# Kernel optimization log

Hardware: AMD Instinct MI355X
Metric: run time of the kernel (lower is better)

## Reference

```python
import jax, jax.numpy as jnp
import numpy as np

B, C1, C2, H, W = 8, 256, 512, 56, 56

def setup_inputs() -> dict:
    key = jax.random.key(0)
    k1, k2, k3, k4, k5 = jax.random.split(key, 5)
    return {
        "x1": jax.random.normal(k1, (B, C1, H, W), dtype=jnp.float32),
        "x2": jax.random.normal(k2, (B, C2, H, W), dtype=jnp.float32),
        "W_proj": jax.random.normal(k3, (C1, C2), dtype=jnp.float32) * (1.0 / np.sqrt(C2)),
        "b_proj": jax.random.normal(k4, (C1,), dtype=jnp.float32) * 0.01,
        "gamma": jax.random.normal(k5, (1,), dtype=jnp.float32) * 0.1,
    }

def reference(x1, x2, W_proj, b_proj, gamma):
    b, c, h, w = x1.shape
    n = h * w
    # 1x1 conv projection C2 -> C1
    x2p = jnp.einsum('oc,bchw->bohw', W_proj, x2) + b_proj[None, :, None, None]
    query = x1.reshape(b, c, n).transpose(0, 2, 1)   # [B, N, C]
    key_ = x2p.reshape(b, c, n)                      # [B, C, N]
    value = x2p.reshape(b, c, n).transpose(0, 2, 1)  # [B, N, C]
    energy = jnp.einsum('bnc,bcm->bnm', query, key_)  # [B, N, N]
    # inverted-energy softmax: max - energy, then softmax over last dim
    energy_new = jnp.max(energy, axis=-1, keepdims=True) - energy
    attention = jax.nn.softmax(energy_new, axis=-1)
    out = jnp.einsum('bnm,bmc->bnc', attention, value)  # [B, N, C]
    out = out.transpose(0, 2, 1).reshape(b, c, h, w)
    return gamma[0] * out + x1
```

## Files before the change

### kernel.cpp

```cpp
#include <hip/hip_runtime.h>
#include <hip/hip_bf16.h>

#define C1 256
#define C2 512
#define NSP 3136
#define NT 98
#define LOG2E 1.44269504f
#define THR2 11.5453f

typedef __attribute__((ext_vector_type(8))) short bf16x8;
typedef __attribute__((ext_vector_type(4))) float f32x4;

__device__ __forceinline__ ushort f2b(float f) {
  __hip_bfloat16 h = __float2bfloat16(f);
  return *reinterpret_cast<ushort*>(&h);
}
__device__ __forceinline__ float b2f(ushort u) {
  union { unsigned int i; float f; } v; v.i = ((unsigned int)u) << 16; return v.f;
}
__device__ __forceinline__ float fexp2(float x) {
  return __builtin_amdgcn_exp2f(x);
}
__device__ __forceinline__ void gload16(const ushort* g, ushort* l) {
  __builtin_amdgcn_global_load_lds(
      (const __attribute__((address_space(1))) void*)g,
      (__attribute__((address_space(3))) void*)l, 16, 0, 0);
}
__device__ __forceinline__ void block_bar() {
  asm volatile("" ::: "memory");
  __builtin_amdgcn_s_barrier();
  asm volatile("" ::: "memory");
}

__global__ __launch_bounds__(256) void k_wtf(const float* __restrict__ W,
                                             ushort* __restrict__ Wf) {
  int ot = blockIdx.x;
  int tid = threadIdx.x;
  int lane = tid & 63, l15 = lane & 15, g = (lane >> 4) & 3;
  int cc0 = (tid >> 6) * 4;
  const float* src = W + (size_t)(ot * 16 + l15) * C2 + g * 8;
#pragma unroll
  for (int k = 0; k < 4; k++) {
    int cc = cc0 + k;
    float4 u0 = *reinterpret_cast<const float4*>(src + cc * 32);
    float4 u1 = *reinterpret_cast<const float4*>(src + cc * 32 + 4);
    bf16x8 v;
    v[0] = (short)f2b(u0.x); v[1] = (short)f2b(u0.y);
    v[2] = (short)f2b(u0.z); v[3] = (short)f2b(u0.w);
    v[4] = (short)f2b(u1.x); v[5] = (short)f2b(u1.y);
    v[6] = (short)f2b(u1.z); v[7] = (short)f2b(u1.w);
    *reinterpret_cast<bf16x8*>(Wf + ((size_t)(ot * 16 + cc)) * 512 + lane * 8) = v;
  }
}

__global__ __launch_bounds__(256) void k_x1t(const float* __restrict__ x1,
                                             ushort* __restrict__ x1t) {
  __shared__ float t[32][33];
  int b = blockIdx.z;
  int n0 = blockIdx.x * 32;
  int c0 = blockIdx.y * 32;
  int tid = threadIdx.x;
  int r = tid >> 3, q = (tid & 7) * 4;
  const float* src = x1 + ((size_t)b * C1 + (c0 + r)) * NSP + n0 + q;
  float4 v = *reinterpret_cast<const float4*>(src);
  t[r][q] = v.x; t[r][q + 1] = v.y; t[r][q + 2] = v.z; t[r][q + 3] = v.w;
  __syncthreads();
  ushort4 o;
  o.x = f2b(t[q + 0][r] * LOG2E); o.y = f2b(t[q + 1][r] * LOG2E);
  o.z = f2b(t[q + 2][r] * LOG2E); o.w = f2b(t[q + 3][r] * LOG2E);
  *reinterpret_cast<ushort4*>(x1t + ((size_t)b * NSP + n0 + r) * C1 + c0 + q) = o;
}

__global__ __launch_bounds__(256) void k_x2f(const float* __restrict__ x2,
                                             ushort* __restrict__ x2f) {
  __shared__ float t[32][33];
  int b = blockIdx.z;
  int n0 = blockIdx.x * 32;
  int cc = blockIdx.y;
  int c0 = cc * 32;
  int tid = threadIdx.x;
  int r = tid >> 3, q = (tid & 7) * 4;
  const float* src = x2 + ((size_t)b * C2 + (c0 + r)) * NSP + n0 + q;
  float4 v = *reinterpret_cast<const float4*>(src);
  t[r][q] = v.x; t[r][q + 1] = v.y; t[r][q + 2] = v.z; t[r][q + 3] = v.w;
  __syncthreads();
  int l15 = tid & 15, g = (tid >> 4) & 3, sub = tid >> 6;
  int ntl = sub & 1, ih = sub >> 1;
  int nl = ntl * 16 + l15;
  int cl = g * 8 + ih * 4;
  ushort4 o;
  o.x = f2b(t[cl + 0][nl]); o.y = f2b(t[cl + 1][nl]);
  o.z = f2b(t[cl + 2][nl]); o.w = f2b(t[cl + 3][nl]);
  int nt16 = (n0 >> 4) + ntl;
  *reinterpret_cast<ushort4*>(
      x2f + (((size_t)b * 196 + nt16) * 16 + cc) * 512 + (size_t)(tid & 63) * 8 + ih * 4) = o;
}

__global__ __launch_bounds__(256) void k_proj(const ushort* __restrict__ Wf,
    const ushort* __restrict__ x2f, const float* __restrict__ bias,
    ushort* __restrict__ Kf, ushort* __restrict__ Vf) {
  __shared__ __align__(16) ushort WL[2][8][512];
  __shared__ __align__(16) ushort XL[2][4][512];
  int bid = blockIdx.x;
  int b = bid & 7;
  int tq = bid >> 3;
  int oh = tq & 1;
  int nt = tq >> 1;
  int tid = threadIdx.x;
  int w = tid >> 6, lane = tid & 63, l15 = lane & 15, g = lane >> 4;
  int wq = w >> 1, wn = w & 1;
  int ot0 = oh * 8;
  int nt0 = nt * 4;

  auto stage = [&](int buf, int cc) {
#pragma unroll
    for (int j = 0; j < 3; j++) {
      int chunk = w * 3 + j;
      if (chunk < 8) {
        gload16(Wf + ((size_t)(ot0 + chunk) * 16 + cc) * 512 + lane * 8,
                &WL[buf][chunk][0]);
      } else {
        gload16(x2f + (((size_t)b * 196 + nt0 + (chunk - 8)) * 16 + cc) * 512 + lane * 8,
                &XL[buf][chunk - 8][0]);
      }
    }
  };

  f32x4 zero = {0.f, 0.f, 0.f, 0.f};
  f32x4 acc[4][2];
#pragma unroll
  for (int a = 0; a < 4; a++)
#pragma unroll
    for (int v = 0; v < 2; v++) acc[a][v] = zero;

  stage(0, 0);
  __syncthreads();

  for (int cc = 0; cc < 16; ++cc) {
    int cur = cc & 1;
    if (cc < 15) stage(cur ^ 1, cc + 1);
    bf16x8 A[4], Bf[2];
#pragma unroll
    for (int a = 0; a < 4; a++)
      A[a] = *reinterpret_cast<const bf16x8*>(&WL[cur][wq * 4 + a][lane * 8]);
#pragma unroll
    for (int v = 0; v < 2; v++)
      Bf[v] = *reinterpret_cast<const bf16x8*>(&XL[cur][wn * 2 + v][lane * 8]);
#pragma unroll
    for (int a = 0; a < 4; a++)
#pragma unroll
      for (int v = 0; v < 2; v++)
        acc[a][v] = __builtin_amdgcn_mfma_f32_16x16x32_bf16(A[a], Bf[v], acc[a][v], 0, 0, 0);
    __syncthreads();
  }

  int obase = oh * 128 + wq * 64;
  float4 bias4[4];
#pragma unroll
  for (int a = 0; a < 4; a++)
    bias4[a] = *reinterpret_cast<const float4*>(&bias[obase + a * 16 + g * 4]);

  int gk = (g & 1) * 4;
#pragma unroll
  for (int a = 0; a < 4; a++) {
    int laneK = (((2 * a + (g >> 1)) & 3) << 4) | l15;
    size_t oK = (size_t)(oh * 4 + wq * 2 + (a >> 1));
#pragma unroll
    for (int v = 0; v < 2; v++) {
      int nK = nt * 4 + wn * 2 + v;
      ushort4 st;
      st.x = f2b(acc[a][v][0] + bias4[a].x);
      st.y = f2b(acc[a][v][1] + bias4[a].y);
      st.z = f2b(acc[a][v][2] + bias4[a].z);
      st.w = f2b(acc[a][v][3] + bias4[a].w);
      *reinterpret_cast<ushort4*>(
          Kf + ((((size_t)b * 196 + nK) * 8 + oK) * 64 + laneK) * 8 + gk) = st;
    }
  }
  int nV = nt * 2 + wn;
#pragma unroll
  for (int v = 0; v < 2; v++) {
    int gv = ((v * 2 + (l15 >> 3)) & 3) << 4;
    int iV = l15 & 7;
#pragma unroll
    for (int a = 0; a < 4; a++) {
      int cs = oh * 8 + wq * 4 + a;
      size_t basev = ((((size_t)b * 98 + nV) * 16 + cs) * 64 + gv) * 8 + iV;
      const float* bp4 = reinterpret_cast<const float*>(&bias4[a]);
#pragma unroll
      for (int r = 0; r < 4; r++)
        Vf[basev + (size_t)(g * 4 + r) * 8] = f2b(acc[a][v][r] + bp4[r]);
    }
  }
}

__global__ __launch_bounds__(256, 3) void k_attn_s(
    const ushort* __restrict__ x1t, const ushort* __restrict__ Kf,
    const ushort* __restrict__ Vf,
    ushort* __restrict__ Po, float* __restrict__ Mv, float* __restrict__ Lv) {
  __shared__ __align__(16) ushort Kt[2][8192];
  __shared__ __align__(16) ushort Vt[8192];
  __shared__ __align__(16) ushort Plds[4][16][36];
  int bid = blockIdx.x;
  int x = bid & 7;
  int j = bid >> 3;
  int s = (4802 * j) / 96;
  int e = (4802 * (j + 1)) / 96;
  int tid = threadIdx.x;
  int w = tid >> 6;
  int lane = tid & 63;
  int l15 = lane & 15;
  int g = lane >> 4;
  int nloc = w * 16 + g * 4;

  const ushort* kg = Kf + (size_t)x * 196 * 8 * 512;
  const ushort* vg = Vf + (size_t)x * 98 * 16 * 512;
  int soff = w * 2048;

  f32x4 zero = {0.f, 0.f, 0.f, 0.f};
  f32x4 O[16];
  f32x4 O17 = zero;
  float M[4];
  bf16x8 qf[8];
  bf16x8 onesf;
#pragma unroll
  for (int i = 0; i < 8; i++) onesf[i] = (short)0x3F80;

  auto resetacc = [&]() {
#pragma unroll
    for (int i = 0; i < 16; i++) O[i] = zero;
    O17 = zero;
#pragma unroll
    for (int r = 0; r < 4; r++) M[r] = -3.0e38f;
  };
  auto loadQ = [&](int u) {
    const ushort* qb = x1t + ((size_t)x * NSP + u * 64 + w * 16 + l15) * C1 + g * 8;
#pragma unroll
    for (int cc = 0; cc < 8; cc++)
      qf[cc] = *reinterpret_cast<const bf16x8*>(qb + cc * 32);
  };

  int u = s / 98;
  int kv = s - u * 98;
  loadQ(u);
  resetacc();
  {
    const ushort* ks = kg + (size_t)kv * 8192 + soff + lane * 8;
#pragma unroll
    for (int jj = 0; jj < 4; ++jj) gload16(ks + jj * 512, &Kt[0][soff] + jj * 512);
  }
  asm volatile("s_waitcnt vmcnt(0)" ::: "memory");
  block_bar();

  int cur = 0;
  for (int i = s; i < e; ++i) {
    {
      const ushort* vs = vg + (size_t)kv * 8192 + soff + lane * 8;
#pragma unroll
      for (int jj = 0; jj < 4; ++jj) gload16(vs + jj * 512, &Vt[soff] + jj * 512);
    }
    asm volatile("" ::: "memory");
    if (i + 1 < e) {
      int kvn = (kv == 97) ? 0 : kv + 1;
      const ushort* ks = kg + (size_t)kvn * 8192 + soff + lane * 8;
#pragma unroll
      for (int jj = 0; jj < 4; ++jj) gload16(ks + jj * 512, &Kt[cur ^ 1][soff] + jj * 512);
    }
    asm volatile("" ::: "memory");

    f32x4 s0a = zero, s0b = zero, s1a = zero, s1b = zero;
    const ushort* kb = &Kt[cur][0];
    __builtin_amdgcn_s_setprio(1);
#pragma unroll
    for (int cc = 0; cc < 8; cc += 2) {
      bf16x8 k00 = *reinterpret_cast<const bf16x8*>(kb + ((size_t)cc * 64 + lane) * 8);
      bf16x8 k10 = *reinterpret_cast<const bf16x8*>(kb + ((size_t)(8 + cc) * 64 + lane) * 8);
      bf16x8 k01 = *reinterpret_cast<const bf16x8*>(kb + ((size_t)(cc + 1) * 64 + lane) * 8);
      bf16x8 k11 = *reinterpret_cast<const bf16x8*>(kb + ((size_t)(9 + cc) * 64 + lane) * 8);
      s0a = __builtin_amdgcn_mfma_f32_16x16x32_bf16(qf[cc], k00, s0a, 0, 0, 0);
      s1a = __builtin_amdgcn_mfma_f32_16x16x32_bf16(qf[cc], k10, s1a, 0, 0, 0);
      s0b = __builtin_amdgcn_mfma_f32_16x16x32_bf16(qf[cc + 1], k01, s0b, 0, 0, 0);
      s1b = __builtin_amdgcn_mfma_f32_16x16x32_bf16(qf[cc + 1], k11, s1b, 0, 0, 0);
    }
    __builtin_amdgcn_s_setprio(0);

    float a0[4], a1[4], tmax[4];
#pragma unroll
    for (int r = 0; r < 4; r++) {
      a0[r] = -(s0a[r] + s0b[r]);
      a1[r] = -(s1a[r] + s1b[r]);
      float mx = fmaxf(a0[r], a1[r]);
      mx = fmaxf(mx, __shfl_xor(mx, 1));
      mx = fmaxf(mx, __shfl_xor(mx, 2));
      mx = fmaxf(mx, __shfl_xor(mx, 4));
      mx = fmaxf(mx, __shfl_xor(mx, 8));
      tmax[r] = mx;
    }
    float d01 = fmaxf(tmax[0] - M[0], tmax[1] - M[1]);
    float d23 = fmaxf(tmax[2] - M[2], tmax[3] - M[3]);
    if (__any(fmaxf(d01, d23) > THR2)) {
      float scv[4];
#pragma unroll
      for (int r = 0; r < 4; r++) {
        float nm = fmaxf(M[r], tmax[r]);
        scv[r] = fexp2(M[r] - nm);
        M[r] = nm;
      }
#pragma unroll
      for (int i2 = 0; i2 < 16; i2++) {
#pragma unroll
        for (int r = 0; r < 4; r++) O[i2][r] *= scv[r];
      }
#pragma unroll
      for (int r = 0; r < 4; r++) O17[r] *= scv[r];
    }
#pragma unroll
    for (int r = 0; r < 4; r++) {
      Plds[w][g * 4 + r][l15] = f2b(fexp2(a0[r] - M[r]));
      Plds[w][g * 4 + r][16 + l15] = f2b(fexp2(a1[r] - M[r]));
    }

    if (i + 1 < e) { asm volatile("s_waitcnt vmcnt(4)" ::: "memory"); }
    else           { asm volatile("s_waitcnt vmcnt(0)" ::: "memory"); }
    block_bar();

    asm volatile("s_waitcnt lgkmcnt(0)" ::: "memory");
    bf16x8 pf = *reinterpret_cast<const bf16x8*>(&Plds[w][l15][g * 8]);
    __builtin_amdgcn_s_setprio(1);
#pragma unroll
    for (int cs = 0; cs < 16; ++cs) {
      bf16x8 vf = *reinterpret_cast<const bf16x8*>(&Vt[0] + ((size_t)cs * 64 + lane) * 8);
      O[cs] = __builtin_amdgcn_mfma_f32_16x16x32_bf16(pf, vf, O[cs], 0, 0, 0);
    }
    O17 = __builtin_amdgcn_mfma_f32_16x16x32_bf16(pf, onesf, O17, 0, 0, 0);
    __builtin_amdgcn_s_setprio(0);

    asm volatile("s_waitcnt vmcnt(0)" ::: "memory");
    block_bar();
    cur ^= 1;

    if ((i + 1 == e) || (kv == 97)) {
      int firstj = (9408 * u + 95) / 4802;
      int slot = (x * 49 + u) * 3 + (j - firstj);
#pragma unroll
      for (int cs = 0; cs < 16; cs++) {
        int c = cs * 16 + l15;
        ushort4 st;
        st.x = f2b(O[cs][0]); st.y = f2b(O[cs][1]);
        st.z = f2b(O[cs][2]); st.w = f2b(O[cs][3]);
        *reinterpret_cast<ushort4*>(Po + ((size_t)slot * 256 + c) * 64 + nloc) = st;
      }
      if (l15 == 0) {
#pragma unroll
        for (int r = 0; r < 4; r++) {
          Mv[(size_t)slot * 64 + nloc + r] = M[r];
          Lv[(size_t)slot * 64 + nloc + r] = O17[r];
        }
      }
      if (i + 1 < e && kv == 97) { u += 1; loadQ(u); resetacc(); }
    }
    kv = (kv == 97) ? 0 : kv + 1;
  }
}

__global__ __launch_bounds__(256) void k_comb3(
    const ushort* __restrict__ Po, const float* __restrict__ Mv,
    const float* __restrict__ Lv, const float* __restrict__ x1,
    const float* __restrict__ gamma, float* __restrict__ out) {
  int bid = blockIdx.x;
  int x = bid & 7;
  int u = bid >> 3;
  int tid = threadIdx.x;
  int n = tid & 63;
  int c0 = (tid >> 6) * 64;
  int firstj = (9408 * u + 95) / 4802;
  int lastj = (96 * (98 * u + 97) + 95) / 4802;
  int np = lastj - firstj + 1;
  size_t base = (size_t)(x * 49 + u) * 3;
  bool has2 = (np >= 3);

  float M0 = Mv[(base + 0) * 64 + n];
  float M1 = Mv[(base + 1) * 64 + n];
  float M2 = has2 ? Mv[(base + 2) * 64 + n] : -3.0e38f;
  float L0 = Lv[(base + 0) * 64 + n];
  float L1 = Lv[(base + 1) * 64 + n];
  float L2 = has2 ? Lv[(base + 2) * 64 + n] : 0.f;
  float Mg = fmaxf(fmaxf(M0, M1), M2);
  float w0 = fexp2(M0 - Mg), w1 = fexp2(M1 - Mg);
  float w2 = has2 ? fexp2(M2 - Mg) : 0.f;
  float rl = gamma[0] / (w0 * L0 + w1 * L1 + w2 * L2);

  const ushort* p0 = Po + ((base + 0) * 256) * 64 + n;
  const ushort* p1 = Po + ((base + 1) * 256) * 64 + n;
  const ushort* p2 = Po + ((base + 2) * 256) * 64 + n;
  size_t ob = (size_t)x * C1 * NSP + u * 64 + n;
#pragma unroll 4
  for (int c = c0; c < c0 + 64; ++c) {
    float acc = w0 * b2f(p0[(size_t)c * 64]) + w1 * b2f(p1[(size_t)c * 64]);
    if (has2) acc += w2 * b2f(p2[(size_t)c * 64]);
    size_t idx = ob + (size_t)c * NSP;
    out[idx] = acc * rl + x1[idx];
  }
}

extern "C" void kernel_launch(void* const* d_in, const int* in_sizes, int n_in,
                              void* d_out, int out_size, void* d_ws, size_t ws_size,
                              hipStream_t stream) {
  const float* x1 = (const float*)d_in[0];
  const float* x2 = (const float*)d_in[1];
  const float* W = (const float*)d_in[2];
  const float* bp = (const float*)d_in[3];
  const float* gamma = (const float*)d_in[4];
  float* out = (float*)d_out;

  char* ws = (char*)d_ws;
  ushort* Wf = (ushort*)(ws + 0);
  ushort* x1t = (ushort*)(ws + 262144);
  ushort* Kf = (ushort*)(ws + 13107200);
  ushort* Vf = (ushort*)(ws + 25952256);
  ushort* Po = (ushort*)(ws + 38797312);
  float* Mv = (float*)(ws + 77332480);
  float* Lv = (float*)(ws + 77633536);
  ushort* x2f = (ushort*)d_out;

  k_wtf<<<dim3(16), dim3(256), 0, stream>>>(W, Wf);
  k_x1t<<<dim3(98, 8, 8), dim3(256), 0, stream>>>(x1, x1t);
  k_x2f<<<dim3(98, 16, 8), dim3(256), 0, stream>>>(x2, x2f);
  k_proj<<<dim3(784), dim3(256), 0, stream>>>(Wf, x2f, bp, Kf, Vf);
  k_attn_s<<<dim3(768), dim3(256), 0, stream>>>(x1t, Kf, Vf, Po, Mv, Lv);
  k_comb3<<<dim3(392), dim3(256), 0, stream>>>(Po, Mv, Lv, x1, gamma, out);
}
```

Before: 238.7 us.

## Partition PV accumulator by channel across waves instead of by query rows

Each wave now owns 4 channel fragments for all 64 query rows, rather than all 256 channels for its own 16 rows. It reads the P tiles of all four waves from LDS and each V fragment once, reusing every V load across four MFMAs. Rescale factors and flags are shared through LDS so any wave's rescale is applied to the right accumulator rows. The aim is to cut V LDS reads per wave fourfold, at the cost of extra P loads, a block-wide rescale condition, and more scattered output stores.

New measurement: 524.6 us. 120% more time.

```diff
diff --git a/kernel.cpp b/kernel.cpp
--- a/kernel.cpp
+++ b/kernel.cpp
@@ -201,6 +201,8 @@
   __shared__ __align__(16) ushort Kt[2][8192];
   __shared__ __align__(16) ushort Vt[8192];
   __shared__ __align__(16) ushort Plds[4][16][36];
+  __shared__ __align__(16) float Sclds[64];
+  __shared__ int Fl[4];
   int bid = blockIdx.x;
   int x = bid & 7;
   int j = bid >> 3;
@@ -296,43 +298,61 @@
       mx = fmaxf(mx, __shfl_xor(mx, 8));
       tmax[r] = mx;
     }
+    float scv[4] = {1.f, 1.f, 1.f, 1.f};
     float d01 = fmaxf(tmax[0] - M[0], tmax[1] - M[1]);
     float d23 = fmaxf(tmax[2] - M[2], tmax[3] - M[3]);
-    if (__any(fmaxf(d01, d23) > THR2)) {
-      float scv[4];
+    int myresc = __any(fmaxf(d01, d23) > THR2) ? 1 : 0;
+    if (myresc) {
 #pragma unroll
       for (int r = 0; r < 4; r++) {
         float nm = fmaxf(M[r], tmax[r]);
         scv[r] = fexp2(M[r] - nm);
         M[r] = nm;
+        O17[r] *= scv[r];
       }
-#pragma unroll
-      for (int i2 = 0; i2 < 16; i2++) {
-#pragma unroll
-        for (int r = 0; r < 4; r++) O[i2][r] *= scv[r];
-      }
-#pragma unroll
-      for (int r = 0; r < 4; r++) O17[r] *= scv[r];
-    }
+    }
+    if (l15 == 0) {
+#pragma unroll
+      for (int r = 0; r < 4; r++) Sclds[w * 16 + g * 4 + r] = scv[r];
+    }
+    if (lane == 0) Fl[w] = myresc;
 #pragma unroll
     for (int r = 0; r < 4; r++) {
       Plds[w][g * 4 + r][l15] = f2b(fexp2(a0[r] - M[r]));
       Plds[w][g * 4 + r][16 + l15] = f2b(fexp2(a1[r] - M[r]));
     }
 
-    if (i + 1 < e) { asm volatile("s_waitcnt vmcnt(4)" ::: "memory"); }
-    else           { asm volatile("s_waitcnt vmcnt(0)" ::: "memory"); }
+    if (i + 1 < e) { asm volatile("s_waitcnt vmcnt(4) lgkmcnt(0)" ::: "memory"); }
+    else           { asm volatile("s_waitcnt vmcnt(0) lgkmcnt(0)" ::: "memory"); }
     block_bar();
 
-    asm volatile("s_waitcnt lgkmcnt(0)" ::: "memory");
-    bf16x8 pf = *reinterpret_cast<const bf16x8*>(&Plds[w][l15][g * 8]);
+    if (Fl[0] | Fl[1] | Fl[2] | Fl[3]) {
+      f32x4 sc[4];
+#pragma unroll
+      for (int rc = 0; rc < 4; rc++)
+        sc[rc] = *reinterpret_cast<const f32x4*>(&Sclds[rc * 16 + g * 4]);
+#pragma unroll
+      for (int cf = 0; cf < 4; cf++)
+#pragma unroll
+        for (int rc = 0; rc < 4; rc++)
+#pragma unroll
+          for (int r = 0; r < 4; r++) O[cf * 4 + rc][r] *= sc[rc][r];
+    }
+
+    bf16x8 pa[4];
+#pragma unroll
+    for (int rc = 0; rc < 4; rc++)
+      pa[rc] = *reinterpret_cast<const bf16x8*>(&Plds[rc][l15][g * 8]);
     __builtin_amdgcn_s_setprio(1);
 #pragma unroll
-    for (int cs = 0; cs < 16; ++cs) {
-      bf16x8 vf = *reinterpret_cast<const bf16x8*>(&Vt[0] + ((size_t)cs * 64 + lane) * 8);
-      O[cs] = __builtin_amdgcn_mfma_f32_16x16x32_bf16(pf, vf, O[cs], 0, 0, 0);
-    }
-    O17 = __builtin_amdgcn_mfma_f32_16x16x32_bf16(pf, onesf, O17, 0, 0, 0);
+    for (int cf = 0; cf < 4; cf++) {
+      bf16x8 vf = *reinterpret_cast<const bf16x8*>(
+          &Vt[0] + ((size_t)(w * 4 + cf) * 64 + lane) * 8);
+#pragma unroll
+      for (int rc = 0; rc < 4; rc++)
+        O[cf * 4 + rc] = __builtin_amdgcn_mfma_f32_16x16x32_bf16(pa[rc], vf, O[cf * 4 + rc], 0, 0, 0);
+    }
+    O17 = __builtin_amdgcn_mfma_f32_16x16x32_bf16(pa[w], onesf, O17, 0, 0, 0);
     __builtin_amdgcn_s_setprio(0);
 
     asm volatile("s_waitcnt vmcnt(0)" ::: "memory");
@@ -343,12 +363,16 @@
       int firstj = (9408 * u + 95) / 4802;
       int slot = (x * 49 + u) * 3 + (j - firstj);
 #pragma unroll
-      for (int cs = 0; cs < 16; cs++) {
-        int c = cs * 16 + l15;
-        ushort4 st;
-        st.x = f2b(O[cs][0]); st.y = f2b(O[cs][1]);
-        st.z = f2b(O[cs][2]); st.w = f2b(O[cs][3]);
-        *reinterpret_cast<ushort4*>(Po + ((size_t)slot * 256 + c) * 64 + nloc) = st;
+      for (int cf = 0; cf < 4; cf++) {
+        int c = (w * 4 + cf) * 16 + l15;
+#pragma unroll
+        for (int rc = 0; rc < 4; rc++) {
+          int n = rc * 16 + g * 4;
+          ushort4 st;
+          st.x = f2b(O[cf * 4 + rc][0]); st.y = f2b(O[cf * 4 + rc][1]);
+          st.z = f2b(O[cf * 4 + rc][2]); st.w = f2b(O[cf * 4 + rc][3]);
+          *reinterpret_cast<ushort4*>(Po + ((size_t)slot * 256 + c) * 64 + n) = st;
+        }
       }
       if (l15 == 0) {
 #pragma unroll
```
